# Kernel tuning notes

Measured on AMD Instinct MI355X. Metric: run time of the kernel, lower is better.

The kernel has to match this reference:

```python
import jax, jax.numpy as jnp
import numpy as np

EPS = 1e-5  # torch GroupNorm default
KNN_K = 16


def _knn_idx(Q, P, K):
    # Q:[B,Nq,3], P:[B,Np,3] -> idx [B,Nq,K], ascending squared distance
    d = (jnp.sum(Q * Q, -1)[:, :, None] + jnp.sum(P * P, -1)[:, None, :]
         - 2.0 * jnp.einsum('bqc,bkc->bqk', Q, P))
    _, idx = jax.lax.top_k(-d, K)
    return idx


def _gather_nbr(feat_bnc, idx_bqk):
    # feat:[B,Np,C], idx:[B,Nq,K] -> [B,Nq,K,C]  (knn_gather)
    return jax.vmap(lambda f, i: f[i])(feat_bnc, idx_bqk)


def _group_norm(x_bcnk, gamma, beta, num_groups=8):
    B, C, N, K = x_bcnk.shape
    G = min(num_groups, C)
    xg = x_bcnk.reshape(B, G, C // G, N, K)
    mu = xg.mean(axis=(2, 3, 4), keepdims=True)
    var = xg.var(axis=(2, 3, 4), keepdims=True)
    xn = ((xg - mu) / jnp.sqrt(var + EPS)).reshape(B, C, N, K)
    return xn * gamma[None, :, None, None] + beta[None, :, None, None]


def _edge_conv(Fq_bcn, Fk_bcn, Pq_b3n, Pk_b3n, k, W, gamma, beta):
    # EdgeConv: concat(x_j - x_i, x_i) -> conv1x1 -> GN -> ReLU -> max over K
    idx = _knn_idx(Pq_b3n.transpose(0, 2, 1), Pk_b3n.transpose(0, 2, 1), k)
    nbr = _gather_nbr(Fk_bcn.transpose(0, 2, 1), idx)          # [B,Nq,K,Cin]
    Fi = jnp.broadcast_to(Fq_bcn.transpose(0, 2, 1)[:, :, None, :], nbr.shape)
    pair = jnp.concatenate([nbr - Fi, Fi], axis=-1)            # [B,Nq,K,2Cin]
    out = jnp.einsum('oc,bnkc->bonk', W, pair)                 # conv 1x1, no bias
    out = _group_norm(out, gamma, beta)
    out = jax.nn.relu(out)
    return out.max(axis=-1)                                    # [B,Cout,Nq]


def _fps_idx(P_b3n, m):
    # Farthest point sampling starting at index 0 (pytorch3d default)
    def one(Pn3):
        d0 = jnp.sum((Pn3 - Pn3[0]) ** 2, -1)
        def step(dists, _):
            nxt = jnp.argmax(dists)
            d = jnp.sum((Pn3 - Pn3[nxt]) ** 2, -1)
            return jnp.minimum(dists, d), nxt
        _, idxs = jax.lax.scan(step, d0, None, length=m - 1)
        return jnp.concatenate([jnp.zeros((1,), jnp.int32), idxs.astype(jnp.int32)])
    return jax.vmap(one)(P_b3n.transpose(0, 2, 1))


def _gather_bcn(x_bcn, idx_bm):
    return jax.vmap(lambda x, i: x[:, i])(x_bcn, idx_bm)


def setup_inputs() -> dict:
    key = jax.random.key(0)
    ks = jax.random.split(key, 8)
    B, N = 2, 8192
    def w(k, shape, s=0.1):
        return jax.random.normal(k, shape, jnp.float32) * s
    return {
        'xyz': jax.random.normal(ks[0], (B, 3, N), jnp.float32),
        'stem_w': w(ks[1], (8, 3)), 'stem_b': jnp.zeros((8,), jnp.float32),
        'w1': w(ks[2], (32, 16)),  'g1': jnp.ones((32,), jnp.float32),  'b1': jnp.zeros((32,), jnp.float32),
        'w2': w(ks[3], (64, 64)),  'g2': jnp.ones((64,), jnp.float32),  'b2': jnp.zeros((64,), jnp.float32),
        'w3': w(ks[4], (64, 128)), 'g3': jnp.ones((64,), jnp.float32),  'b3': jnp.zeros((64,), jnp.float32),
        'w4': w(ks[5], (128, 128)),'g4': jnp.ones((128,), jnp.float32), 'b4': jnp.zeros((128,), jnp.float32),
    }


def reference(xyz, stem_w, stem_b, w1, g1, b1, w2, g2, b2, w3, g3, b3, w4, g4, b4):
    K = KNN_K
    P0 = xyz                                                     # [B,3,N0]
    F0 = jnp.einsum('oc,bcn->bon', stem_w, xyz) + stem_b[None, :, None]
    F0a = _edge_conv(F0, F0, P0, P0, K, w1, g1, b1)              # [B,32,N0]
    N0 = P0.shape[2]
    N1 = max(1, N0 // 4)
    idx1 = _fps_idx(P0, N1)
    P1 = _gather_bcn(P0, idx1)
    F1sk = _gather_bcn(F0a, idx1)
    F1a = _edge_conv(F1sk, F0a, P1, P0, K, w2, g2, b2)           # [B,64,N1]
    N2 = max(1, N1 // 4)
    idx2 = _fps_idx(P1, N2)
    P2 = _gather_bcn(P1, idx2)
    F2sk = _gather_bcn(F1a, idx2)
    F2mid = _edge_conv(F2sk, F1a, P2, P1, K, w3, g3, b3)         # [B,64,N2]
    F2a = _edge_conv(F2mid, F1a, P2, P1, K, w4, g4, b4)          # [B,128,N2]
    return (P0, F0a, P1, F1a, P2, F2a)
```

## Files before the change

### kernel.cpp

```cpp
#include <hip/hip_runtime.h>
#include <math.h>

typedef unsigned long long ull;

__global__ __launch_bounds__(256) void stem_kernel(const float* __restrict__ xyz,
    const float* __restrict__ w, const float* __restrict__ bias,
    float* __restrict__ F0, int N){
  int id = blockIdx.x*256 + threadIdx.x;
  int n = id % N; int b = id / N;
  float x = xyz[((size_t)b*3+0)*N+n];
  float y = xyz[((size_t)b*3+1)*N+n];
  float z = xyz[((size_t)b*3+2)*N+n];
  #pragma unroll
  for (int o=0;o<8;o++){
    float v = fmaf(w[o*3+0],x, fmaf(w[o*3+1],y, fmaf(w[o*3+2],z, bias[o])));
    F0[((size_t)b*8+o)*N+n] = v;
  }
}

__global__ __launch_bounds__(256) void knn_kernel(
    const float* __restrict__ Pq, const float* __restrict__ Pp,
    float* __restrict__ part_d, int* __restrict__ part_i,
    int Nq, int Np, int CAND, int total){
  __shared__ float4 tile[256];
  int qg = blockIdx.x*256 + threadIdx.x;
  int b  = qg / Nq, qn = qg % Nq;
  int s  = blockIdx.y;
  const float* Pqb = Pq + (size_t)b*3*Nq;
  const float* Ppb = Pp + (size_t)b*3*Np;
  float qx = Pqb[qn], qy = Pqb[Nq+qn], qz = Pqb[2*Nq+qn];
  float qq = __fadd_rn(__fadd_rn(__fmul_rn(qx,qx),__fmul_rn(qy,qy)),__fmul_rn(qz,qz));

  float dl[16]; int il[16];
  #pragma unroll
  for (int u=0;u<16;u++){ dl[u]=INFINITY; il[u]=-1; }
  float maxd = INFINITY; int maxslot = 0;

  int c0 = s*CAND;
  for (int tb=0; tb<CAND; tb+=256){
    int p = c0 + tb + threadIdx.x;
    float px = Ppb[p], py = Ppb[Np+p], pz = Ppb[2*Np+p];
    float pp = __fadd_rn(__fadd_rn(__fmul_rn(px,px),__fmul_rn(py,py)),__fmul_rn(pz,pz));
    __syncthreads();
    tile[threadIdx.x] = make_float4(px,py,pz,pp);
    __syncthreads();
    for (int j=0;j<256;j++){
      float4 c = tile[j];
      float dot = __fadd_rn(__fadd_rn(__fmul_rn(qx,c.x),__fmul_rn(qy,c.y)),__fmul_rn(qz,c.z));
      float dc  = __fsub_rn(__fadd_rn(qq,c.w), __fmul_rn(2.0f,dot));
      if (dc < maxd){
        int pidx = c0 + tb + j;
        #pragma unroll
        for (int u=0;u<16;u++){ bool sel=(maxslot==u); dl[u]=sel?dc:dl[u]; il[u]=sel?pidx:il[u]; }
        maxd = dl[0]; maxslot = 0;
        #pragma unroll
        for (int u=1;u<16;u++){ bool g=(dl[u]>maxd); maxd=g?dl[u]:maxd; maxslot=g?u:maxslot; }
      }
    }
  }
  #pragma unroll
  for (int u=0;u<16;u++){
    size_t row = (size_t)(s*16+u);
    part_d[row*total + qg] = dl[u];
    part_i[row*total + qg] = il[u];
  }
}

__global__ __launch_bounds__(256) void knn_merge(const float* __restrict__ part_d,
    const int* __restrict__ part_i, int* __restrict__ idxk, int rows, int total){
  int qg = blockIdx.x*256 + threadIdx.x;
  if (qg >= total) return;
  float dl[16]; int il[16];
  #pragma unroll
  for (int u=0;u<16;u++){ dl[u]=INFINITY; il[u]=0x7fffffff; }
  float maxd = INFINITY; int maxi = 0x7fffffff; int maxslot = 0;
  for (int e=0;e<rows;e++){
    float d = part_d[(size_t)e*total + qg];
    int  ii = part_i[(size_t)e*total + qg];
    bool better = (d < maxd) || (d == maxd && ii < maxi);
    if (better){
      #pragma unroll
      for (int u=0;u<16;u++){ bool sel=(maxslot==u); dl[u]=sel?d:dl[u]; il[u]=sel?ii:il[u]; }
      maxd = dl[0]; maxi = il[0]; maxslot = 0;
      #pragma unroll
      for (int u=1;u<16;u++){
        bool g = (dl[u]>maxd) || (dl[u]==maxd && il[u]>maxi);
        maxd=g?dl[u]:maxd; maxi=g?il[u]:maxi; maxslot=g?u:maxslot;
      }
    }
  }
  #pragma unroll
  for (int u=0;u<16;u++) idxk[(size_t)qg*16+u] = il[u];
}

template<int CIN, int COUT>
__global__ __launch_bounds__(1024) void edge_conv_pre(
    const float* __restrict__ Fk, const float* __restrict__ Fi,
    const int* __restrict__ idx, const float* __restrict__ W,
    float* __restrict__ pre, int Nq, int Np){
  constexpr int C2  = 2*CIN;
  constexpr int PAD = C2 + 4;
  constexpr int TO  = (COUT <= 64) ? COUT : 64;
  constexpr int OP  = COUT / TO;
  extern __shared__ float sm[];
  float* Wl = sm;
  float* Pl = sm + COUT*PAD;
  int t = threadIdx.x;
  int n = blockIdx.x, b = blockIdx.y;
  for (int e=t; e<COUT*C2; e += blockDim.x){
    int o=e/C2, c=e%C2; Wl[o*PAD+c] = W[e];
  }
  const int* idxn = idx + ((size_t)b*Nq + n)*16;
  for (int e=t; e<16*C2; e += blockDim.x){
    int k = e/C2, c = e%C2;
    int cc = (c < CIN) ? c : (c-CIN);
    float fi = Fi[((size_t)b*CIN + cc)*Nq + n];
    float v;
    if (c < CIN){ int nb = idxn[k]; v = Fk[((size_t)b*CIN + c)*Np + nb] - fi; }
    else v = fi;
    Pl[k*PAD+c] = v;
  }
  __syncthreads();
  int k = t & 15, o0 = t >> 4;
  #pragma unroll
  for (int op=0; op<OP; op++){
    int o = o0 + op*TO;
    float acc = 0.f;
    #pragma unroll
    for (int c=0;c<C2;c+=4){
      float4 wv = *(const float4*)&Wl[o*PAD+c];
      float4 pv = *(const float4*)&Pl[k*PAD+c];
      acc = fmaf(wv.x,pv.x,acc); acc = fmaf(wv.y,pv.y,acc);
      acc = fmaf(wv.z,pv.z,acc); acc = fmaf(wv.w,pv.w,acc);
    }
    pre[(((size_t)b*COUT + o)*Nq + n)*16 + k] = acc;
  }
}

__global__ __launch_bounds__(256) void gn_reduce(const float* __restrict__ pre,
    double* __restrict__ gsum, int slabLen){
  int b = blockIdx.z, g = blockIdx.y;
  size_t base = ((size_t)(b*8+g))*slabLen;
  int chunkLen = slabLen / gridDim.x;
  const float* p = pre + base + (size_t)blockIdx.x*chunkLen;
  double s=0.0, sq=0.0;
  for (int i = threadIdx.x*4; i < chunkLen; i += 1024){
    float4 v = *(const float4*)(p+i);
    s += (double)v.x; sq = fma((double)v.x,(double)v.x,sq);
    s += (double)v.y; sq = fma((double)v.y,(double)v.y,sq);
    s += (double)v.z; sq = fma((double)v.z,(double)v.z,sq);
    s += (double)v.w; sq = fma((double)v.w,(double)v.w,sq);
  }
  #pragma unroll
  for (int off=32; off>=1; off>>=1){ s += __shfl_down(s, off); sq += __shfl_down(sq, off); }
  __shared__ double ls[4], lq[4];
  int wid = threadIdx.x>>6;
  if ((threadIdx.x&63)==0){ ls[wid]=s; lq[wid]=sq; }
  __syncthreads();
  if (threadIdx.x==0){
    double S=ls[0]+ls[1]+ls[2]+ls[3], Q=lq[0]+lq[1]+lq[2]+lq[3];
    atomicAdd(&gsum[(b*8+g)*2],   S);
    atomicAdd(&gsum[(b*8+g)*2+1], Q);
  }
}

template<int COUT>
__global__ __launch_bounds__(256) void gn_act_max(const float* __restrict__ pre,
    const double* __restrict__ gsum, const float* __restrict__ gamma,
    const float* __restrict__ beta, float* __restrict__ outF, int Nq){
  int id = blockIdx.x*256 + threadIdx.x;
  int o = (id/Nq)%COUT; int b = id/(Nq*COUT);
  int g = o/(COUT/8);
  double s = gsum[(b*8+g)*2], sq = gsum[(b*8+g)*2+1];
  double cnt = (double)(COUT/8)*Nq*16.0;
  double mu  = s/cnt;
  double var = sq/cnt - mu*mu;
  float muf=(float)mu, rstd=(float)(1.0/sqrt(var+1e-5));
  float ga=gamma[o], be=beta[o];
  const float4* p = (const float4*)(pre + (size_t)id*16);
  float m = 0.f;
  #pragma unroll
  for (int q=0;q<4;q++){
    float4 v = p[q];
    m = fmaxf(m, fmaf((v.x-muf)*rstd, ga, be));
    m = fmaxf(m, fmaf((v.y-muf)*rstd, ga, be));
    m = fmaxf(m, fmaf((v.z-muf)*rstd, ga, be));
    m = fmaxf(m, fmaf((v.w-muf)*rstd, ga, be));
  }
  outF[id] = m;
}

template<int CTRL>
__device__ __forceinline__ float dpp_maxf(float x){
  int y = __builtin_amdgcn_update_dpp(0, __float_as_int(x), CTRL, 0xf, 0xf, true);
  return fmaxf(x, __int_as_float(y));
}

template<int PPT, int BLK, int M>
__global__ __launch_bounds__(BLK, 1) void fps_kernel(const float* __restrict__ P,
    int* __restrict__ idx_out){
  constexpr int N  = PPT*BLK;
  constexpr int NW = BLK/64;
  extern __shared__ __align__(16) float sm[];
  float* lx = sm; float* ly = sm+N; float* lz = sm+2*N;
  ull* wk = (ull*)(sm + 3*N);
  int b = blockIdx.x, t = threadIdx.x;
  const float* Pb = P + (size_t)b*3*N;
  for (int i=t; i<N; i+=BLK){ lx[i]=Pb[i]; ly[i]=Pb[N+i]; lz[i]=Pb[2*N+i]; }
  __syncthreads();
  float px[PPT], py[PPT], pz[PPT], dist[PPT];
  #pragma unroll
  for (int j=0;j<PPT;j++){ int p=t*PPT+j; px[j]=lx[p]; py[j]=ly[p]; pz[j]=lz[p]; }
  #pragma unroll
  for (int j=0;j<PPT;j++){
    asm volatile("" : "+v"(px[j]), "+v"(py[j]), "+v"(pz[j]));
  }
  float sx = lx[0], sy = ly[0], sz = lz[0];
  float bd = -1.f; int bj = 0;
  #pragma unroll
  for (int j=0;j<PPT;j++){
    float dx=__fsub_rn(px[j],sx), dy=__fsub_rn(py[j],sy), dz=__fsub_rn(pz[j],sz);
    float dd=__fadd_rn(__fadd_rn(__fmul_rn(dx,dx),__fmul_rn(dy,dy)),__fmul_rn(dz,dz));
    dist[j]=dd;
    bool c = dd > bd; bd = c?dd:bd; bj = c?j:bj;
  }
  int pbest = t*PPT + bj;
  if (t==0) idx_out[(size_t)b*M] = 0;
  int wid = t>>6, lane = t&63, par = 0;
  for (int i=1;i<M;i++){
    float r = bd;
    r = dpp_maxf<0x111>(r); r = dpp_maxf<0x112>(r);
    r = dpp_maxf<0x114>(r); r = dpp_maxf<0x118>(r);
    r = dpp_maxf<0x142>(r); r = dpp_maxf<0x143>(r);
    float wmax = __int_as_float(__builtin_amdgcn_readlane(__float_as_int(r), 63));
    ull msk = __ballot(bd == wmax);
    int srcl = __ffsll(msk) - 1;
    int wp = __builtin_amdgcn_readlane(pbest, srcl);
    if (lane==0)
      wk[par*NW + wid] = ((ull)__float_as_uint(wmax)<<32)
                       | (unsigned)(~(unsigned)wp);
    __syncthreads();
    ull best = wk[par*NW];
    #pragma unroll
    for (int w=1;w<NW;w++){ ull o = wk[par*NW+w]; best = (o>best)?o:best; }
    unsigned widx = ~(unsigned)best;
    if (t==0) idx_out[(size_t)b*M + i] = (int)widx;
    float nsx = lx[widx], nsy = ly[widx], nsz = lz[widx];
    par ^= 1;
    float nbd = -1.f; int nbj = 0;
    #pragma unroll
    for (int j=0;j<PPT;j++){
      float dx=__fsub_rn(px[j],nsx), dy=__fsub_rn(py[j],nsy), dz=__fsub_rn(pz[j],nsz);
      float dd=__fadd_rn(__fadd_rn(__fmul_rn(dx,dx),__fmul_rn(dy,dy)),__fmul_rn(dz,dz));
      float nd = fminf(dist[j], dd);
      dist[j] = nd;
      bool c = nd > nbd; nbd = c?nd:nbd; nbj = c?j:nbj;
    }
    bd = nbd; pbest = t*PPT + nbj;
  }
}

__global__ __launch_bounds__(256) void gather_kernel(float* __restrict__ dst,
    const float* __restrict__ src, const int* __restrict__ idx,
    int C, int Nsrc, int M){
  int id = blockIdx.x*256 + threadIdx.x;
  int m = id % M; int c = (id/M)%C; int b = id/(M*C);
  dst[id] = src[((size_t)b*C + c)*Nsrc + idx[(size_t)b*M + m]];
}

extern "C" void kernel_launch(void* const* d_in, const int* in_sizes, int n_in,
                              void* d_out, int out_size, void* d_ws, size_t ws_size,
                              hipStream_t stream) {
  const float* xyz    = (const float*)d_in[0];
  const float* stem_w = (const float*)d_in[1];
  const float* stem_b = (const float*)d_in[2];
  const float* w1 = (const float*)d_in[3];
  const float* g1 = (const float*)d_in[4];
  const float* b1 = (const float*)d_in[5];
  const float* w2 = (const float*)d_in[6];
  const float* g2 = (const float*)d_in[7];
  const float* b2 = (const float*)d_in[8];
  const float* w3 = (const float*)d_in[9];
  const float* g3 = (const float*)d_in[10];
  const float* b3 = (const float*)d_in[11];
  const float* w4 = (const float*)d_in[12];
  const float* g4 = (const float*)d_in[13];
  const float* b4 = (const float*)d_in[14];

  float* out = (float*)d_out;
  float* P0o  = out + 0;
  float* F0a  = out + 49152;
  float* P1o  = out + 573440;
  float* F1a  = out + 585728;
  float* P2o  = out + 847872;
  float* F2a  = out + 850944;

  char* ws = (char*)d_ws;
  float* F0     = (float*)(ws + 0);
  float* pre    = (float*)(ws + 524288);
  float* part_d = (float*)(ws + 524288);
  int*   part_i = (int*)  (ws + 524288 + 16777216);
  int*   idxk   = (int*)  (ws + 34078720);
  double* gsum  = (double*)(ws + 35127296);
  int*   idx1   = (int*)  (ws + 35127552);
  int*   idx2   = (int*)  (ws + 35143936);
  float* F1sk   = (float*)(ws + 35148032);
  float* F2sk   = (float*)(ws + 35672320);
  float* F2mid  = (float*)(ws + 35934464);

  size_t smem_c1 = (size_t)(32*20  + 16*20 )*4;
  size_t smem_c2 = (size_t)(64*68  + 16*68 )*4;
  size_t smem_c3 = (size_t)(64*132 + 16*132)*4;
  size_t smem_c4 = (size_t)(128*132+ 16*132)*4;
  size_t smem_f1 = (size_t)3*8192*4 + 256;
  size_t smem_f2 = (size_t)3*2048*4 + 256;

  hipMemcpyAsync(P0o, xyz, (size_t)49152*4, hipMemcpyDeviceToDevice, stream);
  stem_kernel<<<(2*8192)/256, 256, 0, stream>>>(xyz, stem_w, stem_b, F0, 8192);

  knn_kernel<<<dim3(16384/256, 16), 256, 0, stream>>>(xyz, xyz, part_d, part_i, 8192, 8192, 512, 16384);
  knn_merge <<<16384/256, 256, 0, stream>>>(part_d, part_i, idxk, 256, 16384);
  edge_conv_pre<8,32><<<dim3(8192,2), 512, smem_c1, stream>>>(F0, F0, idxk, w1, pre, 8192, 8192);
  hipMemsetAsync(gsum, 0, 256, stream);
  gn_reduce<<<dim3(8,8,2), 256, 0, stream>>>(pre, gsum, 4*8192*16);
  gn_act_max<32><<<(2*32*8192)/256, 256, 0, stream>>>(pre, gsum, g1, b1, F0a, 8192);

  fps_kernel<32,256,2048><<<2, 256, smem_f1, stream>>>(xyz, idx1);
  gather_kernel<<<(2*3*2048)/256, 256, 0, stream>>>(P1o, xyz, idx1, 3, 8192, 2048);
  gather_kernel<<<(2*32*2048)/256, 256, 0, stream>>>(F1sk, F0a, idx1, 32, 8192, 2048);

  knn_kernel<<<dim3(4096/256, 16), 256, 0, stream>>>(P1o, xyz, part_d, part_i, 2048, 8192, 512, 4096);
  knn_merge <<<4096/256, 256, 0, stream>>>(part_d, part_i, idxk, 256, 4096);
  edge_conv_pre<32,64><<<dim3(2048,2), 1024, smem_c2, stream>>>(F0a, F1sk, idxk, w2, pre, 2048, 8192);
  hipMemsetAsync(gsum, 0, 256, stream);
  gn_reduce<<<dim3(4,8,2), 256, 0, stream>>>(pre, gsum, 8*2048*16);
  gn_act_max<64><<<(2*64*2048)/256, 256, 0, stream>>>(pre, gsum, g2, b2, F1a, 2048);

  fps_kernel<8,256,512><<<2, 256, smem_f2, stream>>>(P1o, idx2);
  gather_kernel<<<(2*3*512)/256, 256, 0, stream>>>(P2o, P1o, idx2, 3, 2048, 512);
  gather_kernel<<<(2*64*512)/256, 256, 0, stream>>>(F2sk, F1a, idx2, 64, 2048, 512);

  knn_kernel<<<dim3(1024/256, 8), 256, 0, stream>>>(P2o, P1o, part_d, part_i, 512, 2048, 256, 1024);
  knn_merge <<<1024/256, 256, 0, stream>>>(part_d, part_i, idxk, 128, 1024);
  edge_conv_pre<64,64><<<dim3(512,2), 1024, smem_c3, stream>>>(F1a, F2sk, idxk, w3, pre, 512, 2048);
  hipMemsetAsync(gsum, 0, 256, stream);
  gn_reduce<<<dim3(1,8,2), 256, 0, stream>>>(pre, gsum, 8*512*16);
  gn_act_max<64><<<(2*64*512)/256, 256, 0, stream>>>(pre, gsum, g3, b3, F2mid, 512);

  edge_conv_pre<64,128><<<dim3(512,2), 1024, smem_c4, stream>>>(F1a, F2mid, idxk, w4, pre, 512, 2048);
  hipMemsetAsync(gsum, 0, 256, stream);
  gn_reduce<<<dim3(2,8,2), 256, 0, stream>>>(pre, gsum, 16*512*16);
  gn_act_max<128><<<(2*128*512)/256, 256, 0, stream>>>(pre, gsum, g4, b4, F2a, 512);

  (void)in_sizes; (void)n_in; (void)out_size; (void)ws_size;
}
```

Before: 3.702 ms.

## Fuse kNN with merge, GroupNorm reduce with activation, gathers, and stem copy

Result: faster. 3.484 ms (-5.9%).

```diff
diff --git a/kernel.cpp b/kernel.cpp
--- a/kernel.cpp
+++ b/kernel.cpp
@@ -3,14 +3,17 @@
 
 typedef unsigned long long ull;
 
-__global__ __launch_bounds__(256) void stem_kernel(const float* __restrict__ xyz,
+__global__ __launch_bounds__(256) void stem_fused(const float* __restrict__ xyz,
     const float* __restrict__ w, const float* __restrict__ bias,
-    float* __restrict__ F0, int N){
+    float* __restrict__ F0, float* __restrict__ P0o, int N){
   int id = blockIdx.x*256 + threadIdx.x;
   int n = id % N; int b = id / N;
   float x = xyz[((size_t)b*3+0)*N+n];
   float y = xyz[((size_t)b*3+1)*N+n];
   float z = xyz[((size_t)b*3+2)*N+n];
+  P0o[((size_t)b*3+0)*N+n] = x;
+  P0o[((size_t)b*3+1)*N+n] = y;
+  P0o[((size_t)b*3+2)*N+n] = z;
   #pragma unroll
   for (int o=0;o<8;o++){
     float v = fmaf(w[o*3+0],x, fmaf(w[o*3+1],y, fmaf(w[o*3+2],z, bias[o])));
@@ -18,14 +21,15 @@
   }
 }
 
-__global__ __launch_bounds__(256) void knn_kernel(
+__global__ __launch_bounds__(256) void knn_fused(
     const float* __restrict__ Pq, const float* __restrict__ Pp,
-    float* __restrict__ part_d, int* __restrict__ part_i,
-    int Nq, int Np, int CAND, int total){
-  __shared__ float4 tile[256];
-  int qg = blockIdx.x*256 + threadIdx.x;
-  int b  = qg / Nq, qn = qg % Nq;
-  int s  = blockIdx.y;
+    int* __restrict__ idxk, int Nq, int Np){
+  __shared__ float4 tile[4][256];
+  __shared__ float  pd[16][4][64];
+  __shared__ int    pi[16][4][64];
+  int t = threadIdx.x, w = t>>6, l = t&63;
+  int b = blockIdx.y;
+  int qn = blockIdx.x*64 + l;
   const float* Pqb = Pq + (size_t)b*3*Nq;
   const float* Ppb = Pp + (size_t)b*3*Np;
   float qx = Pqb[qn], qy = Pqb[Nq+qn], qz = Pqb[2*Nq+qn];
@@ -36,16 +40,20 @@
   for (int u=0;u<16;u++){ dl[u]=INFINITY; il[u]=-1; }
   float maxd = INFINITY; int maxslot = 0;
 
-  int c0 = s*CAND;
-  for (int tb=0; tb<CAND; tb+=256){
-    int p = c0 + tb + threadIdx.x;
-    float px = Ppb[p], py = Ppb[Np+p], pz = Ppb[2*Np+p];
-    float pp = __fadd_rn(__fadd_rn(__fmul_rn(px,px),__fmul_rn(py,py)),__fmul_rn(pz,pz));
+  int CANDS = Np >> 2;
+  int c0 = w*CANDS;
+  for (int tb=0; tb<CANDS; tb+=256){
     __syncthreads();
-    tile[threadIdx.x] = make_float4(px,py,pz,pp);
+    #pragma unroll
+    for (int k=0;k<4;k++){
+      int p = c0 + tb + k*64 + l;
+      float px = Ppb[p], py = Ppb[Np+p], pz = Ppb[2*Np+p];
+      float pp = __fadd_rn(__fadd_rn(__fmul_rn(px,px),__fmul_rn(py,py)),__fmul_rn(pz,pz));
+      tile[w][k*64+l] = make_float4(px,py,pz,pp);
+    }
     __syncthreads();
     for (int j=0;j<256;j++){
-      float4 c = tile[j];
+      float4 c = tile[w][j];
       float dot = __fadd_rn(__fadd_rn(__fmul_rn(qx,c.x),__fmul_rn(qy,c.y)),__fmul_rn(qz,c.z));
       float dc  = __fsub_rn(__fadd_rn(qq,c.w), __fmul_rn(2.0f,dot));
       if (dc < maxd){
@@ -59,38 +67,35 @@
     }
   }
   #pragma unroll
-  for (int u=0;u<16;u++){
-    size_t row = (size_t)(s*16+u);
-    part_d[row*total + qg] = dl[u];
-    part_i[row*total + qg] = il[u];
-  }
-}
-
-__global__ __launch_bounds__(256) void knn_merge(const float* __restrict__ part_d,
-    const int* __restrict__ part_i, int* __restrict__ idxk, int rows, int total){
-  int qg = blockIdx.x*256 + threadIdx.x;
-  if (qg >= total) return;
-  float dl[16]; int il[16];
-  #pragma unroll
-  for (int u=0;u<16;u++){ dl[u]=INFINITY; il[u]=0x7fffffff; }
-  float maxd = INFINITY; int maxi = 0x7fffffff; int maxslot = 0;
-  for (int e=0;e<rows;e++){
-    float d = part_d[(size_t)e*total + qg];
-    int  ii = part_i[(size_t)e*total + qg];
-    bool better = (d < maxd) || (d == maxd && ii < maxi);
-    if (better){
+  for (int u=0;u<16;u++){ pd[u][w][l]=dl[u]; pi[u][w][l]=il[u]; }
+  __syncthreads();
+  if (t < 64){
+    int q = t;
+    float mdl[16]; int mil[16];
+    #pragma unroll
+    for (int u=0;u<16;u++){ mdl[u]=INFINITY; mil[u]=0x7fffffff; }
+    float mmaxd = INFINITY; int mmaxi = 0x7fffffff; int mslot = 0;
+    for (int s=0;s<4;s++){
       #pragma unroll
-      for (int u=0;u<16;u++){ bool sel=(maxslot==u); dl[u]=sel?d:dl[u]; il[u]=sel?ii:il[u]; }
-      maxd = dl[0]; maxi = il[0]; maxslot = 0;
-      #pragma unroll
-      for (int u=1;u<16;u++){
-        bool g = (dl[u]>maxd) || (dl[u]==maxd && il[u]>maxi);
-        maxd=g?dl[u]:maxd; maxi=g?il[u]:maxi; maxslot=g?u:maxslot;
+      for (int u=0;u<16;u++){
+        float d = pd[u][s][q]; int ii = pi[u][s][q];
+        bool better = (d < mmaxd) || (d == mmaxd && ii < mmaxi);
+        if (better){
+          #pragma unroll
+          for (int v=0;v<16;v++){ bool sel=(mslot==v); mdl[v]=sel?d:mdl[v]; mil[v]=sel?ii:mil[v]; }
+          mmaxd = mdl[0]; mmaxi = mil[0]; mslot = 0;
+          #pragma unroll
+          for (int v=1;v<16;v++){
+            bool g = (mdl[v]>mmaxd) || (mdl[v]==mmaxd && mil[v]>mmaxi);
+            mmaxd=g?mdl[v]:mmaxd; mmaxi=g?mil[v]:mmaxi; mslot=g?v:mslot;
+          }
+        }
       }
     }
-  }
-  #pragma unroll
-  for (int u=0;u<16;u++) idxk[(size_t)qg*16+u] = il[u];
+    #pragma unroll
+    for (int u=0;u<16;u++)
+      idxk[((size_t)b*Nq + blockIdx.x*64 + q)*16 + u] = mil[u];
+  }
 }
 
 template<int CIN, int COUT>
@@ -137,14 +142,17 @@
   }
 }
 
-__global__ __launch_bounds__(256) void gn_reduce(const float* __restrict__ pre,
-    double* __restrict__ gsum, int slabLen){
-  int b = blockIdx.z, g = blockIdx.y;
-  size_t base = ((size_t)(b*8+g))*slabLen;
-  int chunkLen = slabLen / gridDim.x;
-  const float* p = pre + base + (size_t)blockIdx.x*chunkLen;
+template<int COUT>
+__global__ __launch_bounds__(1024) void gn_fused(const float* __restrict__ pre,
+    const float* __restrict__ gamma, const float* __restrict__ beta,
+    float* __restrict__ outF, int Nq){
+  constexpr int CPG = COUT/8;
+  int g = blockIdx.x, b = blockIdx.y, t = threadIdx.x;
+  size_t base = (((size_t)b*COUT + g*CPG)*(size_t)Nq)*16;
+  const float* p = pre + base;
+  int len = CPG*Nq*16;
   double s=0.0, sq=0.0;
-  for (int i = threadIdx.x*4; i < chunkLen; i += 1024){
+  for (int i = t*4; i < len; i += 4096){
     float4 v = *(const float4*)(p+i);
     s += (double)v.x; sq = fma((double)v.x,(double)v.x,sq);
     s += (double)v.y; sq = fma((double)v.y,(double)v.y,sq);
@@ -153,41 +161,40 @@
   }
   #pragma unroll
   for (int off=32; off>=1; off>>=1){ s += __shfl_down(s, off); sq += __shfl_down(sq, off); }
-  __shared__ double ls[4], lq[4];
-  int wid = threadIdx.x>>6;
-  if ((threadIdx.x&63)==0){ ls[wid]=s; lq[wid]=sq; }
-  __syncthreads();
-  if (threadIdx.x==0){
-    double S=ls[0]+ls[1]+ls[2]+ls[3], Q=lq[0]+lq[1]+lq[2]+lq[3];
-    atomicAdd(&gsum[(b*8+g)*2],   S);
-    atomicAdd(&gsum[(b*8+g)*2+1], Q);
-  }
-}
-
-template<int COUT>
-__global__ __launch_bounds__(256) void gn_act_max(const float* __restrict__ pre,
-    const double* __restrict__ gsum, const float* __restrict__ gamma,
-    const float* __restrict__ beta, float* __restrict__ outF, int Nq){
-  int id = blockIdx.x*256 + threadIdx.x;
-  int o = (id/Nq)%COUT; int b = id/(Nq*COUT);
-  int g = o/(COUT/8);
-  double s = gsum[(b*8+g)*2], sq = gsum[(b*8+g)*2+1];
-  double cnt = (double)(COUT/8)*Nq*16.0;
-  double mu  = s/cnt;
-  double var = sq/cnt - mu*mu;
-  float muf=(float)mu, rstd=(float)(1.0/sqrt(var+1e-5));
-  float ga=gamma[o], be=beta[o];
-  const float4* p = (const float4*)(pre + (size_t)id*16);
-  float m = 0.f;
-  #pragma unroll
-  for (int q=0;q<4;q++){
-    float4 v = p[q];
-    m = fmaxf(m, fmaf((v.x-muf)*rstd, ga, be));
-    m = fmaxf(m, fmaf((v.y-muf)*rstd, ga, be));
-    m = fmaxf(m, fmaf((v.z-muf)*rstd, ga, be));
-    m = fmaxf(m, fmaf((v.w-muf)*rstd, ga, be));
-  }
-  outF[id] = m;
+  __shared__ double ls[16], lq[16];
+  __shared__ float stats[2];
+  int wid = t>>6;
+  if ((t&63)==0){ ls[wid]=s; lq[wid]=sq; }
+  __syncthreads();
+  if (t==0){
+    double S=0.0, Q=0.0;
+    #pragma unroll
+    for (int w=0;w<16;w++){ S+=ls[w]; Q+=lq[w]; }
+    double cnt = (double)CPG*(double)Nq*16.0;
+    double mu  = S/cnt;
+    double var = Q/cnt - mu*mu;
+    stats[0] = (float)mu;
+    stats[1] = (float)(1.0/sqrt(var+1e-5));
+  }
+  __syncthreads();
+  float muf = stats[0], rstd = stats[1];
+  int outs = CPG*Nq;
+  for (int e=t; e<outs; e+=1024){
+    int ol = e/Nq, n = e - ol*Nq;
+    int o = g*CPG + ol;
+    float ga = gamma[o], be = beta[o];
+    const float4* pp = (const float4*)(p + (size_t)e*16);
+    float m = 0.f;
+    #pragma unroll
+    for (int q=0;q<4;q++){
+      float4 v = pp[q];
+      m = fmaxf(m, fmaf((v.x-muf)*rstd, ga, be));
+      m = fmaxf(m, fmaf((v.y-muf)*rstd, ga, be));
+      m = fmaxf(m, fmaf((v.z-muf)*rstd, ga, be));
+      m = fmaxf(m, fmaf((v.w-muf)*rstd, ga, be));
+    }
+    outF[((size_t)b*COUT + o)*Nq + n] = m;
+  }
 }
 
 template<int CTRL>
@@ -260,12 +267,22 @@
   }
 }
 
-__global__ __launch_bounds__(256) void gather_kernel(float* __restrict__ dst,
-    const float* __restrict__ src, const int* __restrict__ idx,
-    int C, int Nsrc, int M){
-  int id = blockIdx.x*256 + threadIdx.x;
-  int m = id % M; int c = (id/M)%C; int b = id/(M*C);
-  dst[id] = src[((size_t)b*C + c)*Nsrc + idx[(size_t)b*M + m]];
+__global__ __launch_bounds__(256) void gather_fused(float* __restrict__ Pdst,
+    const float* __restrict__ Psrc, float* __restrict__ Fdst,
+    const float* __restrict__ Fsrc, const int* __restrict__ idxv,
+    int CF, int Nsrc, int M){
+  int per = (3+CF)*M;
+  int total = 2*per;
+  for (int id = blockIdx.x*256 + threadIdx.x; id < total; id += gridDim.x*256){
+    int b = id/per, r = id%per, c = r/M, m = r%M;
+    int sn = idxv[(size_t)b*M + m];
+    if (c < 3)
+      Pdst[((size_t)b*3+c)*M+m] = Psrc[((size_t)b*3+c)*Nsrc+sn];
+    else {
+      int cf = c-3;
+      Fdst[((size_t)b*CF+cf)*M+m] = Fsrc[((size_t)b*CF+cf)*Nsrc+sn];
+    }
+  }
 }
 
 extern "C" void kernel_launch(void* const* d_in, const int* in_sizes, int n_in,
@@ -298,15 +315,12 @@
   char* ws = (char*)d_ws;
   float* F0     = (float*)(ws + 0);
   float* pre    = (float*)(ws + 524288);
-  float* part_d = (float*)(ws + 524288);
-  int*   part_i = (int*)  (ws + 524288 + 16777216);
   int*   idxk   = (int*)  (ws + 34078720);
-  double* gsum  = (double*)(ws + 35127296);
-  int*   idx1   = (int*)  (ws + 35127552);
-  int*   idx2   = (int*)  (ws + 35143936);
-  float* F1sk   = (float*)(ws + 35148032);
-  float* F2sk   = (float*)(ws + 35672320);
-  float* F2mid  = (float*)(ws + 35934464);
+  int*   idx1   = (int*)  (ws + 35127296);
+  int*   idx2   = (int*)  (ws + 35143680);
+  float* F1sk   = (float*)(ws + 35147776);
+  float* F2sk   = (float*)(ws + 35672064);
+  float* F2mid  = (float*)(ws + 35934208);
 
   size_t smem_c1 = (size_t)(32*20  + 16*20 )*4;
   size_t smem_c2 = (size_t)(64*68  + 16*68 )*4;
@@ -315,42 +329,27 @@
   size_t smem_f1 = (size_t)3*8192*4 + 256;
   size_t smem_f2 = (size_t)3*2048*4 + 256;
 
-  hipMemcpyAsync(P0o, xyz, (size_t)49152*4, hipMemcpyDeviceToDevice, stream);
-  stem_kernel<<<(2*8192)/256, 256, 0, stream>>>(xyz, stem_w, stem_b, F0, 8192);
-
-  knn_kernel<<<dim3(16384/256, 16), 256, 0, stream>>>(xyz, xyz, part_d, part_i, 8192, 8192, 512, 16384);
-  knn_merge <<<16384/256, 256, 0, stream>>>(part_d, part_i, idxk, 256, 16384);
+  stem_fused<<<64, 256, 0, stream>>>(xyz, stem_w, stem_b, F0, P0o, 8192);
+  knn_fused<<<dim3(128,2), 256, 0, stream>>>(xyz, xyz, idxk, 8192, 8192);
   edge_conv_pre<8,32><<<dim3(8192,2), 512, smem_c1, stream>>>(F0, F0, idxk, w1, pre, 8192, 8192);
-  hipMemsetAsync(gsum, 0, 256, stream);
-  gn_reduce<<<dim3(8,8,2), 256, 0, stream>>>(pre, gsum, 4*8192*16);
-  gn_act_max<32><<<(2*32*8192)/256, 256, 0, stream>>>(pre, gsum, g1, b1, F0a, 8192);
+  gn_fused<32><<<dim3(8,2), 1024, 0, stream>>>(pre, g1, b1, F0a, 8192);
 
   fps_kernel<32,256,2048><<<2, 256, smem_f1, stream>>>(xyz, idx1);
-  gather_kernel<<<(2*3*2048)/256, 256, 0, stream>>>(P1o, xyz, idx1, 3, 8192, 2048);
-  gather_kernel<<<(2*32*2048)/256, 256, 0, stream>>>(F1sk, F0a, idx1, 32, 8192, 2048);
-
-  knn_kernel<<<dim3(4096/256, 16), 256, 0, stream>>>(P1o, xyz, part_d, part_i, 2048, 8192, 512, 4096);
-  knn_merge <<<4096/256, 256, 0, stream>>>(part_d, part_i, idxk, 256, 4096);
+  gather_fused<<<560, 256, 0, stream>>>(P1o, xyz, F1sk, F0a, idx1, 32, 8192, 2048);
+
+  knn_fused<<<dim3(32,2), 256, 0, stream>>>(P1o, xyz, idxk, 2048, 8192);
   edge_conv_pre<32,64><<<dim3(2048,2), 1024, smem_c2, stream>>>(F0a, F1sk, idxk, w2, pre, 2048, 8192);
-  hipMemsetAsync(gsum, 0, 256, stream);
-  gn_reduce<<<dim3(4,8,2), 256, 0, stream>>>(pre, gsum, 8*2048*16);
-  gn_act_max<64><<<(2*64*2048)/256, 256, 0, stream>>>(pre, gsum, g2, b2, F1a, 2048);
+  gn_fused<64><<<dim3(8,2), 1024, 0, stream>>>(pre, g2, b2, F1a, 2048);
 
   fps_kernel<8,256,512><<<2, 256, smem_f2, stream>>>(P1o, idx2);
-  gather_kernel<<<(2*3*512)/256, 256, 0, stream>>>(P2o, P1o, idx2, 3, 2048, 512);
-  gather_kernel<<<(2*64*512)/256, 256, 0, stream>>>(F2sk, F1a, idx2, 64, 2048, 512);
-
-  knn_kernel<<<dim3(1024/256, 8), 256, 0, stream>>>(P2o, P1o, part_d, part_i, 512, 2048, 256, 1024);
-  knn_merge <<<1024/256, 256, 0, stream>>>(part_d, part_i, idxk, 128, 1024);
+  gather_fused<<<268, 256, 0, stream>>>(P2o, P1o, F2sk, F1a, idx2, 64, 2048, 512);
+
+  knn_fused<<<dim3(8,2), 256, 0, stream>>>(P2o, P1o, idxk, 512, 2048);
   edge_conv_pre<64,64><<<dim3(512,2), 1024, smem_c3, stream>>>(F1a, F2sk, idxk, w3, pre, 512, 2048);
-  hipMemsetAsync(gsum, 0, 256, stream);
-  gn_reduce<<<dim3(1,8,2), 256, 0, stream>>>(pre, gsum, 8*512*16);
-  gn_act_max<64><<<(2*64*512)/256, 256, 0, stream>>>(pre, gsum, g3, b3, F2mid, 512);
+  gn_fused<64><<<dim3(8,2), 1024, 0, stream>>>(pre, g3, b3, F2mid, 512);
 
   edge_conv_pre<64,128><<<dim3(512,2), 1024, smem_c4, stream>>>(F1a, F2mid, idxk, w4, pre, 512, 2048);
-  hipMemsetAsync(gsum, 0, 256, stream);
-  gn_reduce<<<dim3(2,8,2), 256, 0, stream>>>(pre, gsum, 16*512*16);
-  gn_act_max<128><<<(2*128*512)/256, 256, 0, stream>>>(pre, gsum, g4, b4, F2a, 512);
+  gn_fused<128><<<dim3(8,2), 1024, 0, stream>>>(pre, g4, b4, F2a, 512);
 
   (void)in_sizes; (void)n_in; (void)out_size; (void)ws_size;
 }
```
